# Kernel tuning notes

Measured on AMD Instinct MI355X. Metric: run time of the kernel, lower is better.

## Reference

```python
import jax, jax.numpy as jnp
import numpy as np

N = 100_000      # nodes
E = 3_200_000    # edges
B = 1024         # graphs in batch
IN = 4           # in_channels
G = 16           # GCNNodes
D = 32           # NDenseNodes


def _linear_params(k, out_f, in_f):
    s = 1.0 / np.sqrt(in_f)
    kw, kb = jax.random.split(k)
    W = jax.random.uniform(kw, (out_f, in_f), jnp.float32, -s, s)
    b = jax.random.uniform(kb, (out_f,), jnp.float32, -s, s)
    return W, b


def setup_inputs() -> dict:
    key = jax.random.key(0)
    ks = jax.random.split(key, 12)
    X = jax.random.normal(ks[0], (N, IN), jnp.float32)
    Edge_index = jax.random.randint(ks[1], (2, E), 0, N, jnp.int64)
    Edge_weight = jax.random.uniform(ks[2], (E,), jnp.float32)
    Batching = jnp.sort(jax.random.randint(ks[3], (N,), 0, B, jnp.int64))
    W1, b1 = _linear_params(ks[4], G, IN)   # Conv1 lin (PyG GCNConv: Linear no bias + bias param)
    W2, b2 = _linear_params(ks[5], G, G)    # Conv2
    C1w, C1b = _linear_params(ks[6], D, 2 * G)
    C2w, C2b = _linear_params(ks[7], D, D)
    C3w, C3b = _linear_params(ks[8], 1, D)
    R1w, R1b = _linear_params(ks[9], D, 2 * G)
    R2w, R2b = _linear_params(ks[10], D, D)
    R3w, R3b = _linear_params(ks[11], 1, D)
    return {"X": X, "Edge_index": Edge_index, "Edge_weight": Edge_weight,
            "Batching": Batching, "num_graphs": B,
            "W1": W1, "b1": b1, "W2": W2, "b2": b2,
            "C1w": C1w, "C1b": C1b, "C2w": C2w, "C2b": C2b, "C3w": C3w, "C3b": C3b,
            "R1w": R1w, "R1b": R1b, "R2w": R2w, "R2b": R2b, "R3w": R3w, "R3b": R3b}


def _gcn_conv(x, row, col, w, W, b):
    """PyG GCNConv: add self loops (weight 1), symmetric norm, x@W.T, scatter-add at col, +b."""
    n = x.shape[0]
    loop = jnp.arange(n)
    row2 = jnp.concatenate([row, loop])
    col2 = jnp.concatenate([col, loop])
    w2 = jnp.concatenate([w, jnp.ones((n,), x.dtype)])
    deg = jax.ops.segment_sum(w2, col2, num_segments=n)          # deg >= 1 via self loops
    dinv = jnp.where(deg > 0, jax.lax.rsqrt(deg), 0.0)
    norm = dinv[row2] * w2 * dinv[col2]                           # [E+n]
    xw = x @ W.T                                                  # [n, out]
    out = jax.ops.segment_sum(norm[:, None] * xw[row2], col2, num_segments=n)
    return out + b


def reference(X, Edge_index, Edge_weight, Batching, num_graphs,
              W1, b1, W2, b2, C1w, C1b, C2w, C2b, C3w, C3b,
              R1w, R1b, R2w, R2b, R3w, R3b):
    act = jax.nn.leaky_relu  # default slope 0.01, matches nn.LeakyReLU()
    row, col = Edge_index[0], Edge_index[1]
    # add_self_loops then keep only col > row  ==  zero out weights where col <= row
    w = jnp.where(col > row, Edge_weight, 0.0)

    out = act(_gcn_conv(X, row, col, w, W1, b1))
    out = act(_gcn_conv(out, row, col, w, W2, b2))

    ones = jnp.ones((out.shape[0],), out.dtype)
    cnt = jax.ops.segment_sum(ones, Batching, num_segments=num_graphs)
    outMean = jax.ops.segment_sum(out, Batching, num_segments=num_graphs) / jnp.maximum(cnt, 1.0)[:, None]
    outMax = jax.ops.segment_max(out, Batching, num_segments=num_graphs)
    pooled = jnp.concatenate([outMean, outMax], axis=1)           # [B, 2G]

    Chi0 = act(pooled @ C1w.T + C1b)
    Chi0 = act(Chi0 @ C2w.T + C2b)
    Chi0 = Chi0 @ C3w.T + C3b
    Rp = act(pooled @ R1w.T + R1b)
    Rp = act(Rp @ R2w.T + R2b)
    Rp = Rp @ R3w.T + R3b
    return jnp.concatenate([Chi0, Rp], axis=1)                    # [B, 2]
```

## Files before the change

### kernel.cpp

```cpp
#include <hip/hip_runtime.h>
#include <hip/hip_bf16.h>
#include <float.h>

#define LRELU(x) ((x) > 0.0f ? (x) : 0.01f * (x))

typedef unsigned int u32;
typedef unsigned long long u64;

#define WSUM_ONE   (1u << 17)
#define WSUM_MASK  ((1u << 25) - 1)
#define CNT_ONE    (1u << 25)

__global__ __launch_bounds__(256) void k_zero(u32* __restrict__ deg32, int N) {
    int i = blockIdx.x * blockDim.x + threadIdx.x;
    if (i < N) deg32[i] = WSUM_ONE;
}

__global__ __launch_bounds__(256) void k_countx(const int* __restrict__ row,
                                                const int* __restrict__ col,
                                                const float* __restrict__ w,
                                                const float* __restrict__ X,
                                                const float* __restrict__ W1,
                                                u32* __restrict__ deg32,
                                                unsigned char* __restrict__ rank,
                                                float* __restrict__ xw1,
                                                int E, int N, int gE) {
    int tid = threadIdx.x;
    if ((int)blockIdx.x < gE) {
        int e = blockIdx.x * 256 + tid;
        if (e >= E) return;
        int r = row[e], c = col[e];
        if (c <= r) return;
        u32 add = CNT_ONE | (u32)(w[e] * 131072.0f);
        u32 old = atomicAdd(deg32 + c, add);
        rank[e] = (unsigned char)(old >> 25);
    } else {
        int i = (blockIdx.x - gE) * 256 + tid;
        if (i >= N) return;
        const float4 x = *reinterpret_cast<const float4*>(X + 4 * i);
        float o[16];
#pragma unroll
        for (int g = 0; g < 16; ++g) {
            const float4 wr = *reinterpret_cast<const float4*>(W1 + 4 * g);
            o[g] = x.x * wr.x + x.y * wr.y + x.z * wr.z + x.w * wr.w;
        }
        float4* dst = reinterpret_cast<float4*>(xw1 + 16 * i);
#pragma unroll
        for (int k = 0; k < 4; ++k)
            dst[k] = make_float4(o[4 * k], o[4 * k + 1], o[4 * k + 2], o[4 * k + 3]);
    }
}

__global__ __launch_bounds__(256) void k_scan1(const u32* __restrict__ deg32,
                                               int* __restrict__ offs,
                                               int* __restrict__ partials,
                                               float* __restrict__ dinv,
                                               float* __restrict__ xw, int N) {
    __shared__ int sm[256];
    int tid = threadIdx.x;
    int base = blockIdx.x * 1024 + tid * 4;
    int v[4];
    float dv[4];
    int s = 0;
#pragma unroll
    for (int k = 0; k < 4; ++k) {
        int idx = base + k;
        u32 d = (idx < N) ? deg32[idx] : WSUM_ONE;
        v[k] = (int)(d >> 25);
        dv[k] = rsqrtf((float)(d & WSUM_MASK) * (1.0f / 131072.0f));
        s += v[k];
    }
    if (base + 3 < N) {
        *reinterpret_cast<float4*>(dinv + base) = make_float4(dv[0], dv[1], dv[2], dv[3]);
#pragma unroll
        for (int k = 0; k < 4; ++k) {
            float4* p = reinterpret_cast<float4*>(xw + 16 * (base + k));
            float sc = dv[k];
#pragma unroll
            for (int q = 0; q < 4; ++q) {
                float4 t = p[q];
                p[q] = make_float4(sc * t.x, sc * t.y, sc * t.z, sc * t.w);
            }
        }
    } else {
#pragma unroll
        for (int k = 0; k < 4; ++k) {
            if (base + k < N) {
                dinv[base + k] = dv[k];
                float4* p = reinterpret_cast<float4*>(xw + 16 * (base + k));
                float sc = dv[k];
#pragma unroll
                for (int q = 0; q < 4; ++q) {
                    float4 t = p[q];
                    p[q] = make_float4(sc * t.x, sc * t.y, sc * t.z, sc * t.w);
                }
            }
        }
    }
    sm[tid] = s;
    __syncthreads();
    for (int off = 1; off < 256; off <<= 1) {
        int t = (tid >= off) ? sm[tid - off] : 0;
        __syncthreads();
        sm[tid] += t;
        __syncthreads();
    }
    int run = sm[tid] - s;
#pragma unroll
    for (int k = 0; k < 4; ++k) {
        int idx = base + k;
        if (idx < N) offs[idx] = run;
        run += v[k];
    }
    if (tid == 255) partials[blockIdx.x] = sm[255];
}

__global__ __launch_bounds__(256) void k_scan2(int* __restrict__ partials,
                                               int* __restrict__ offs, int nb, int N) {
    __shared__ int sm[256];
    int tid = threadIdx.x;
    int v = (tid < nb) ? partials[tid] : 0;
    sm[tid] = v;
    __syncthreads();
    for (int off = 1; off < 256; off <<= 1) {
        int t = (tid >= off) ? sm[tid - off] : 0;
        __syncthreads();
        sm[tid] += t;
        __syncthreads();
    }
    if (tid < nb) partials[tid] = sm[tid] - v;
    if (tid == nb - 1) offs[N] = sm[tid];
}

__global__ __launch_bounds__(256) void k_fillx(const int* __restrict__ row,
                                               const int* __restrict__ col,
                                               const float* __restrict__ w,
                                               const int* __restrict__ offs,
                                               const int* __restrict__ part,
                                               const unsigned char* __restrict__ rank,
                                               int2* __restrict__ pack,
                                               int* __restrict__ offsF,
                                               int E, int N, int gE) {
    int tid = threadIdx.x;
    if ((int)blockIdx.x < gE) {
        int e = blockIdx.x * 256 + tid;
        if (e >= E) return;
        int r = row[e], c = col[e];
        if (c <= r) return;
        int pos = offs[c] + part[c >> 10] + (int)rank[e];
        pack[pos] = make_int2(r, __float_as_int(w[e]));
    } else {
        int i = (blockIdx.x - gE) * 256 + tid;
        if (i == 0) offsF[N] = offs[N];
        if (i >= N) return;
        offsF[i] = offs[i] + part[i >> 10];
    }
}

__global__ __launch_bounds__(256) void k_gather1m(const int* __restrict__ offsF,
                                                  const int2* __restrict__ pack,
                                                  const float* __restrict__ xs1,
                                                  const float* __restrict__ dinv,
                                                  const float* __restrict__ b1,
                                                  const float* __restrict__ W2,
                                                  float* __restrict__ xs2, int N) {
    int t = blockIdx.x * blockDim.x + threadIdx.x;
    int NT = 16 * N;
    bool valid = t < NT;
    int tc = valid ? t : NT - 1;
    int c = tc >> 4, g = tc & 15;
    int beg = offsF[c], end = offsF[c + 1];
    float d = dinv[c];
    float s = xs1[tc];
    for (int j = beg; j < end; ++j) {
        int2 p = pack[j];
        s += __int_as_float(p.y) * xs1[((size_t)p.x << 4) + g];
    }
    float h = d * s + b1[g];
    h = LRELU(h);
    int lane = threadIdx.x & 63;
    int base = lane & 48;
    const float4* W2r = reinterpret_cast<const float4*>(W2 + 16 * g);
    float4 w0 = W2r[0], w1 = W2r[1], w2 = W2r[2], w3 = W2r[3];
    float o = 0.0f;
    o += __shfl(h, base + 0) * w0.x;
    o += __shfl(h, base + 1) * w0.y;
    o += __shfl(h, base + 2) * w0.z;
    o += __shfl(h, base + 3) * w0.w;
    o += __shfl(h, base + 4) * w1.x;
    o += __shfl(h, base + 5) * w1.y;
    o += __shfl(h, base + 6) * w1.z;
    o += __shfl(h, base + 7) * w1.w;
    o += __shfl(h, base + 8) * w2.x;
    o += __shfl(h, base + 9) * w2.y;
    o += __shfl(h, base + 10) * w2.z;
    o += __shfl(h, base + 11) * w2.w;
    o += __shfl(h, base + 12) * w3.x;
    o += __shfl(h, base + 13) * w3.y;
    o += __shfl(h, base + 14) * w3.z;
    o += __shfl(h, base + 15) * w3.w;
    if (valid) xs2[t] = d * o;
}

__global__ __launch_bounds__(256) void k_gather2(const int* __restrict__ offsF,
                                                 const int2* __restrict__ pack,
                                                 const float* __restrict__ xs2,
                                                 const float* __restrict__ dinv,
                                                 const float* __restrict__ b2,
                                                 float* __restrict__ acc, int N) {
    int t = blockIdx.x * blockDim.x + threadIdx.x;
    if (t >= 16 * N) return;
    int c = t >> 4, g = t & 15;
    int beg = offsF[c], end = offsF[c + 1];
    float d = dinv[c];
    float s = xs2[t];
    for (int j = beg; j < end; ++j) {
        int2 p = pack[j];
        s += __int_as_float(p.y) * xs2[((size_t)p.x << 4) + g];
    }
    float a = d * s + b2[g];
    acc[t] = LRELU(a);
}

__global__ __launch_bounds__(64) void k_poolA(const float* __restrict__ acc,
                                              const int* __restrict__ batching,
                                              int N,
                                              const float* __restrict__ C1w, const float* __restrict__ C1b,
                                              const float* __restrict__ C2w, const float* __restrict__ C2b,
                                              const float* __restrict__ C3w, const float* __restrict__ C3b,
                                              const float* __restrict__ R1w, const float* __restrict__ R1b,
                                              const float* __restrict__ R2w, const float* __restrict__ R2b,
                                              const float* __restrict__ R3w, const float* __restrict__ R3b,
                                              float* __restrict__ out) {
    int b = blockIdx.x;
    int t = threadIdx.x;
    __shared__ int s_se[2];
    __shared__ float sp[32];
    __shared__ float h1s[64];
    __shared__ float h2s[64];
    if (t < 2) {
        int target = b + t;
        int lo = 0, hi = N;
        while (lo < hi) {
            int mid = (lo + hi) >> 1;
            if (batching[mid] < target) lo = mid + 1; else hi = mid;
        }
        s_se[t] = lo;
    }
    __syncthreads();
    int start = s_se[0], end = s_se[1];
    int g = t & 15, sub = t >> 4;
    float sum = 0.0f, mx = -FLT_MAX;
    for (int n = start + sub; n < end; n += 4) {
        float v = acc[16 * n + g];
        sum += v;
        mx = fmaxf(mx, v);
    }
    sum += __shfl_down(sum, 32);
    mx = fmaxf(mx, __shfl_down(mx, 32));
    sum += __shfl_down(sum, 16);
    mx = fmaxf(mx, __shfl_down(mx, 16));
    if (t < 16) {
        float cnt = (float)(end - start);
        sp[t] = sum / fmaxf(cnt, 1.0f);
        sp[16 + t] = mx;
    }
    __syncthreads();
    int d = t & 31;
    const float* W1h = (t < 32) ? C1w : R1w;
    const float* b1h = (t < 32) ? C1b : R1b;
    float a1 = b1h[d];
#pragma unroll 4
    for (int k = 0; k < 32; ++k) a1 += sp[k] * W1h[32 * d + k];
    h1s[t] = LRELU(a1);
    __syncthreads();
    const float* W2h = (t < 32) ? C2w : R2w;
    const float* b2h = (t < 32) ? C2b : R2b;
    const float* h1base = h1s + (t < 32 ? 0 : 32);
    float a2 = b2h[d];
#pragma unroll 4
    for (int k = 0; k < 32; ++k) a2 += h1base[k] * W2h[32 * d + k];
    h2s[t] = LRELU(a2);
    __syncthreads();
    if (t == 0 || t == 32) {
        const float* w3 = (t == 0) ? C3w : R3w;
        float a3 = (t == 0) ? C3b[0] : R3b[0];
        const float* hb = h2s + t;
#pragma unroll 4
        for (int k = 0; k < 32; ++k) a3 += hb[k] * w3[k];
        out[2 * b + (t >> 5)] = a3;
    }
}

__global__ __launch_bounds__(256) void k_initf(const float* __restrict__ X,
                                               const float* __restrict__ W1,
                                               float* __restrict__ deg,
                                               float* __restrict__ xw, int N) {
    int i = blockIdx.x * blockDim.x + threadIdx.x;
    if (i >= N) return;
    deg[i] = 1.0f;
    const float4 x = *reinterpret_cast<const float4*>(X + 4 * i);
    float o[16];
#pragma unroll
    for (int g = 0; g < 16; ++g) {
        const float4 wr = *reinterpret_cast<const float4*>(W1 + 4 * g);
        o[g] = x.x * wr.x + x.y * wr.y + x.z * wr.z + x.w * wr.w;
    }
    float4* dst = reinterpret_cast<float4*>(xw + 16 * i);
#pragma unroll
    for (int k = 0; k < 4; ++k)
        dst[k] = make_float4(o[4 * k], o[4 * k + 1], o[4 * k + 2], o[4 * k + 3]);
}

__global__ __launch_bounds__(256) void k_degf(const int* __restrict__ row,
                                              const int* __restrict__ col,
                                              const float* __restrict__ w,
                                              float* __restrict__ deg, int E) {
    int e = blockIdx.x * blockDim.x + threadIdx.x;
    if (e >= E) return;
    int r = row[e], c = col[e];
    if (c > r) atomicAdd(deg + c, w[e]);
}

__global__ __launch_bounds__(256) void k_self(float* __restrict__ deg_dinv,
                                              const float* __restrict__ xw,
                                              float* __restrict__ acc, int N) {
    int i = blockIdx.x * blockDim.x + threadIdx.x;
    if (i >= N) return;
    float d = rsqrtf(deg_dinv[i]);
    deg_dinv[i] = d;
    float s = d * d;
    const float4* xs = reinterpret_cast<const float4*>(xw + 16 * i);
    float4* as = reinterpret_cast<float4*>(acc + 16 * i);
#pragma unroll
    for (int k = 0; k < 4; ++k) {
        float4 v = xs[k];
        as[k] = make_float4(s * v.x, s * v.y, s * v.z, s * v.w);
    }
}

__global__ __launch_bounds__(256) void k_scatter(const int* __restrict__ row,
                                                 const int* __restrict__ col,
                                                 const float* __restrict__ w,
                                                 const float* __restrict__ dinv,
                                                 const float* __restrict__ xw,
                                                 float* __restrict__ acc, int E) {
    int e = blockIdx.x * blockDim.x + threadIdx.x;
    if (e >= E) return;
    int r = row[e], c = col[e];
    if (c <= r) return;
    float nrm = dinv[r] * w[e] * dinv[c];
    const float4* xr = reinterpret_cast<const float4*>(xw + 16 * r);
    float* ac = acc + 16 * c;
#pragma unroll
    for (int k = 0; k < 4; ++k) {
        float4 v = xr[k];
        atomicAdd(ac + 4 * k + 0, nrm * v.x);
        atomicAdd(ac + 4 * k + 1, nrm * v.y);
        atomicAdd(ac + 4 * k + 2, nrm * v.z);
        atomicAdd(ac + 4 * k + 3, nrm * v.w);
    }
}

__global__ __launch_bounds__(256) void k_mid(const float* __restrict__ b1,
                                             const float* __restrict__ W2,
                                             const float* __restrict__ dinv,
                                             float* __restrict__ xw,
                                             float* __restrict__ acc, int N) {
    int i = blockIdx.x * blockDim.x + threadIdx.x;
    if (i >= N) return;
    float h[16];
#pragma unroll
    for (int g = 0; g < 16; ++g) {
        float v = acc[16 * i + g] + b1[g];
        h[g] = LRELU(v);
    }
    float d = dinv[i];
    float s = d * d;
#pragma unroll
    for (int g = 0; g < 16; ++g) {
        float a = 0.0f;
#pragma unroll
        for (int k = 0; k < 16; ++k) a += h[k] * W2[16 * g + k];
        xw[16 * i + g] = a;
        acc[16 * i + g] = s * a;
    }
}

__global__ __launch_bounds__(256) void k_act(const float* __restrict__ b2,
                                             float* __restrict__ acc, int NT) {
    int t = blockIdx.x * blockDim.x + threadIdx.x;
    if (t >= NT) return;
    float v = acc[t] + b2[t & 15];
    acc[t] = LRELU(v);
}

extern "C" void kernel_launch(void* const* d_in, const int* in_sizes, int n_in,
                              void* d_out, int out_size, void* d_ws, size_t ws_size,
                              hipStream_t stream) {
    const float* X   = (const float*)d_in[0];
    const int*   EI  = (const int*)d_in[1];
    const float* EW  = (const float*)d_in[2];
    const int*   Bat = (const int*)d_in[3];
    const float* W1  = (const float*)d_in[5];
    const float* b1  = (const float*)d_in[6];
    const float* W2  = (const float*)d_in[7];
    const float* b2  = (const float*)d_in[8];
    const float* C1w = (const float*)d_in[9];
    const float* C1b = (const float*)d_in[10];
    const float* C2w = (const float*)d_in[11];
    const float* C2b = (const float*)d_in[12];
    const float* C3w = (const float*)d_in[13];
    const float* C3b = (const float*)d_in[14];
    const float* R1w = (const float*)d_in[15];
    const float* R1b = (const float*)d_in[16];
    const float* R2w = (const float*)d_in[17];
    const float* R2b = (const float*)d_in[18];
    const float* R3w = (const float*)d_in[19];
    const float* R3b = (const float*)d_in[20];

    const int N = in_sizes[0] / 4;
    const int E = in_sizes[1] / 2;
    const int B = out_size / 2;
    const int* row = EI;
    const int* col = EI + E;

    float* outp = (float*)d_out;

    const int CAP = E / 2 + 16384;

    size_t off = 0;
    u32*   deg32 = (u32*)d_ws;            off += (size_t)N;
    float* xs1   = (float*)d_ws + off;    off += 16 * (size_t)N;
    float* xs2   = (float*)d_ws + off;    off += 16 * (size_t)N;
    float* dinv  = (float*)d_ws + off;    off += (size_t)N;
    int*   offs  = (int*)d_ws + off;      off += (size_t)N + 1;
    int*   offsF = (int*)d_ws + off;      off += (size_t)N + 1;
    int*   part  = (int*)d_ws + off;      off += 256;
    unsigned char* rank = (unsigned char*)((int*)d_ws + off);
    off += ((size_t)E + 3) / 4;
    off = (off + 1) & ~(size_t)1;
    int2*  pack  = (int2*)((int*)d_ws + off); off += 2 * (size_t)CAP;
    size_t needed = off * 4;

    const int nb = (N + 1023) / 1024;

    dim3 blk(256);
    const int gN  = (N + 255) / 256;
    const int gE  = (E + 255) / 256;
    const int gNG = (16 * N + 255) / 256;

    if (needed <= ws_size && nb <= 256) {
        float* acc = xs1;
        k_zero  <<<dim3(gN), blk, 0, stream>>>(deg32, N);
        k_countx<<<dim3(gE + gN), blk, 0, stream>>>(row, col, EW, X, W1,
                                                    deg32, rank, xs1, E, N, gE);
        k_scan1 <<<dim3(nb), blk, 0, stream>>>(deg32, offs, part, dinv, xs1, N);
        k_scan2 <<<dim3(1), blk, 0, stream>>>(part, offs, nb, N);
        k_fillx <<<dim3(gE + gN), blk, 0, stream>>>(row, col, EW, offs, part,
                                                    rank, pack, offsF, E, N, gE);
        k_gather1m<<<dim3(gNG), blk, 0, stream>>>(offsF, pack, xs1, dinv, b1, W2, xs2, N);
        k_gather2 <<<dim3(gNG), blk, 0, stream>>>(offsF, pack, xs2, dinv, b2, acc, N);
        k_poolA <<<dim3(B), dim3(64), 0, stream>>>(acc, Bat, N,
                                                   C1w, C1b, C2w, C2b, C3w, C3b,
                                                   R1w, R1b, R2w, R2b, R3w, R3b,
                                                   outp);
    } else {
        float* deg = (float*)d_ws;
        float* xw  = (float*)d_ws + N;
        float* acc = xw + 16 * (size_t)N;
        k_initf<<<dim3(gN), blk, 0, stream>>>(X, W1, deg, xw, N);
        k_degf <<<dim3(gE), blk, 0, stream>>>(row, col, EW, deg, E);
        k_self <<<dim3(gN), blk, 0, stream>>>(deg, xw, acc, N);
        k_scatter<<<dim3(gE), blk, 0, stream>>>(row, col, EW, deg, xw, acc, E);
        k_mid  <<<dim3(gN), blk, 0, stream>>>(b1, W2, deg, xw, acc, N);
        k_scatter<<<dim3(gE), blk, 0, stream>>>(row, col, EW, deg, xw, acc, E);
        k_act  <<<dim3(gNG), blk, 0, stream>>>(b2, acc, 16 * N);
        k_poolA<<<dim3(B), dim3(64), 0, stream>>>(acc, Bat, N,
                                                  C1w, C1b, C2w, C2b, C3w, C3b,
                                                  R1w, R1b, R2w, R2b, R3w, R3b,
                                                  outp);
    }
}
```

Before: 240.6 us.

## Pack CSR edges into 32-bit words with quantized weights and precomputed metadata

Edge entries in the CSR pack shrink from an int2 (row, float weight) to a single 32-bit word holding a 17-bit source index and a 15-bit fixed-point weight. The count pass also writes per-edge metadata (target column and rank) and the packed word, so the fill pass no longer rereads row, col and weight. The degree-buffer init kernel is replaced by a memset, with the self-loop contribution added during the scan. This cuts gather bandwidth but quantizes edge weights and limits node count to 2^17, and adds extra per-edge writes in the count pass.

```diff
diff --git a/kernel.cpp b/kernel.cpp
--- a/kernel.cpp
+++ b/kernel.cpp
@@ -7,14 +7,9 @@
 typedef unsigned int u32;
 typedef unsigned long long u64;
 
-#define WSUM_ONE   (1u << 17)
 #define WSUM_MASK  ((1u << 25) - 1)
 #define CNT_ONE    (1u << 25)
-
-__global__ __launch_bounds__(256) void k_zero(u32* __restrict__ deg32, int N) {
-    int i = blockIdx.x * blockDim.x + threadIdx.x;
-    if (i < N) deg32[i] = WSUM_ONE;
-}
+#define META_INV   0xFFFFFFFFu
 
 __global__ __launch_bounds__(256) void k_countx(const int* __restrict__ row,
                                                 const int* __restrict__ col,
@@ -22,7 +17,8 @@
                                                 const float* __restrict__ X,
                                                 const float* __restrict__ W1,
                                                 u32* __restrict__ deg32,
-                                                unsigned char* __restrict__ rank,
+                                                u32* __restrict__ meta,
+                                                u32* __restrict__ cpk,
                                                 float* __restrict__ xw1,
                                                 int E, int N, int gE) {
     int tid = threadIdx.x;
@@ -30,10 +26,17 @@
         int e = blockIdx.x * 256 + tid;
         if (e >= E) return;
         int r = row[e], c = col[e];
-        if (c <= r) return;
-        u32 add = CNT_ONE | (u32)(w[e] * 131072.0f);
-        u32 old = atomicAdd(deg32 + c, add);
-        rank[e] = (unsigned char)(old >> 25);
+        if (c > r) {
+            float wv = w[e];
+            u32 q15 = (u32)(wv * 32768.0f);
+            if (q15 > 32767u) q15 = 32767u;
+            u32 add = CNT_ONE | (u32)(wv * 131072.0f);
+            u32 old = atomicAdd(deg32 + c, add);
+            meta[e] = ((u32)c << 7) | (old >> 25);
+            cpk[e]  = ((u32)r << 15) | q15;
+        } else {
+            meta[e] = META_INV;
+        }
     } else {
         int i = (blockIdx.x - gE) * 256 + tid;
         if (i >= N) return;
@@ -65,9 +68,9 @@
 #pragma unroll
     for (int k = 0; k < 4; ++k) {
         int idx = base + k;
-        u32 d = (idx < N) ? deg32[idx] : WSUM_ONE;
+        u32 d = (idx < N) ? deg32[idx] : 0u;
         v[k] = (int)(d >> 25);
-        dv[k] = rsqrtf((float)(d & WSUM_MASK) * (1.0f / 131072.0f));
+        dv[k] = rsqrtf(1.0f + (float)(d & WSUM_MASK) * (1.0f / 131072.0f));
         s += v[k];
     }
     if (base + 3 < N) {
@@ -132,23 +135,22 @@
     if (tid == nb - 1) offs[N] = sm[tid];
 }
 
-__global__ __launch_bounds__(256) void k_fillx(const int* __restrict__ row,
-                                               const int* __restrict__ col,
-                                               const float* __restrict__ w,
+__global__ __launch_bounds__(256) void k_fillx(const u32* __restrict__ meta,
+                                               const u32* __restrict__ cpk,
                                                const int* __restrict__ offs,
                                                const int* __restrict__ part,
-                                               const unsigned char* __restrict__ rank,
-                                               int2* __restrict__ pack,
+                                               u32* __restrict__ pack,
                                                int* __restrict__ offsF,
                                                int E, int N, int gE) {
     int tid = threadIdx.x;
     if ((int)blockIdx.x < gE) {
         int e = blockIdx.x * 256 + tid;
         if (e >= E) return;
-        int r = row[e], c = col[e];
-        if (c <= r) return;
-        int pos = offs[c] + part[c >> 10] + (int)rank[e];
-        pack[pos] = make_int2(r, __float_as_int(w[e]));
+        u32 m = meta[e];
+        if (m == META_INV) return;
+        int c = (int)(m >> 7);
+        int pos = offs[c] + part[c >> 10] + (int)(m & 127u);
+        pack[pos] = cpk[e];
     } else {
         int i = (blockIdx.x - gE) * 256 + tid;
         if (i == 0) offsF[N] = offs[N];
@@ -158,7 +160,7 @@
 }
 
 __global__ __launch_bounds__(256) void k_gather1m(const int* __restrict__ offsF,
-                                                  const int2* __restrict__ pack,
+                                                  const u32* __restrict__ pack,
                                                   const float* __restrict__ xs1,
                                                   const float* __restrict__ dinv,
                                                   const float* __restrict__ b1,
@@ -173,8 +175,8 @@
     float d = dinv[c];
     float s = xs1[tc];
     for (int j = beg; j < end; ++j) {
-        int2 p = pack[j];
-        s += __int_as_float(p.y) * xs1[((size_t)p.x << 4) + g];
+        u32 p = pack[j];
+        s += (float)(p & 32767u) * (1.0f / 32768.0f) * xs1[(((size_t)(p >> 15)) << 4) + g];
     }
     float h = d * s + b1[g];
     h = LRELU(h);
@@ -203,7 +205,7 @@
 }
 
 __global__ __launch_bounds__(256) void k_gather2(const int* __restrict__ offsF,
-                                                 const int2* __restrict__ pack,
+                                                 const u32* __restrict__ pack,
                                                  const float* __restrict__ xs2,
                                                  const float* __restrict__ dinv,
                                                  const float* __restrict__ b2,
@@ -215,8 +217,8 @@
     float d = dinv[c];
     float s = xs2[t];
     for (int j = beg; j < end; ++j) {
-        int2 p = pack[j];
-        s += __int_as_float(p.y) * xs2[((size_t)p.x << 4) + g];
+        u32 p = pack[j];
+        s += (float)(p & 32767u) * (1.0f / 32768.0f) * xs2[(((size_t)(p >> 15)) << 4) + g];
     }
     float a = d * s + b2[g];
     acc[t] = LRELU(a);
@@ -437,10 +439,9 @@
     int*   offs  = (int*)d_ws + off;      off += (size_t)N + 1;
     int*   offsF = (int*)d_ws + off;      off += (size_t)N + 1;
     int*   part  = (int*)d_ws + off;      off += 256;
-    unsigned char* rank = (unsigned char*)((int*)d_ws + off);
-    off += ((size_t)E + 3) / 4;
-    off = (off + 1) & ~(size_t)1;
-    int2*  pack  = (int2*)((int*)d_ws + off); off += 2 * (size_t)CAP;
+    u32*   meta  = (u32*)d_ws + off;      off += (size_t)E;
+    u32*   cpk   = (u32*)d_ws + off;      off += (size_t)E;
+    u32*   pack  = (u32*)d_ws + off;      off += (size_t)CAP;
     size_t needed = off * 4;
 
     const int nb = (N + 1023) / 1024;
@@ -452,13 +453,13 @@
 
     if (needed <= ws_size && nb <= 256) {
         float* acc = xs1;
-        k_zero  <<<dim3(gN), blk, 0, stream>>>(deg32, N);
+        hipMemsetAsync(deg32, 0, (size_t)N * sizeof(u32), stream);
         k_countx<<<dim3(gE + gN), blk, 0, stream>>>(row, col, EW, X, W1,
-                                                    deg32, rank, xs1, E, N, gE);
+                                                    deg32, meta, cpk, xs1, E, N, gE);
         k_scan1 <<<dim3(nb), blk, 0, stream>>>(deg32, offs, part, dinv, xs1, N);
         k_scan2 <<<dim3(1), blk, 0, stream>>>(part, offs, nb, N);
-        k_fillx <<<dim3(gE + gN), blk, 0, stream>>>(row, col, EW, offs, part,
-                                                    rank, pack, offsF, E, N, gE);
+        k_fillx <<<dim3(gE + gN), blk, 0, stream>>>(meta, cpk, offs, part,
+                                                    pack, offsF, E, N, gE);
         k_gather1m<<<dim3(gNG), blk, 0, stream>>>(offsF, pack, xs1, dinv, b1, W2, xs2, N);
         k_gather2 <<<dim3(gNG), blk, 0, stream>>>(offsF, pack, xs2, dinv, b2, acc, N);
         k_poolA <<<dim3(B), dim3(64), 0, stream>>>(acc, Bat, N,
```

Result: no change. 236.6 us (-1.7%).
